# Performance work log

Hardware: AMD Instinct MI355X
Metric: run time of the kernel (lower is better)

Reference implementation:

```python
import jax, jax.numpy as jnp
import numpy as np

EPS = 1e-5
PI = np.pi
HPK_SCL = 4.0  # args.hpk_scl

def _nan_to(y, rep):
    return jnp.where(jnp.isnan(y), rep, y)

def _chi(x):
    return _nan_to(1.0 / jnp.sqrt(1.0 + PI * jnp.tan(x + EPS) ** 2), 0.0)

def _E1(x, th):
    return _nan_to(jnp.exp(-(2.0 / PI) / jnp.tan(th + EPS) / jnp.tan(x + EPS)), 0.0)

def _E2(x, th):
    return _nan_to(jnp.exp(-(1.0 / PI) * (1.0 / jnp.tan(th + EPS)) ** 2 * (1.0 / jnp.tan(x + EPS)) ** 2), 0.0)

def _eta(x, th):
    y = _chi(th) * (jnp.cos(x) + jnp.sin(x) * jnp.tan(th + EPS) * (_E2(x, th) / (2.0 - _E1(x, th))))
    return _nan_to(y, 0.0)

def _f(phi):
    return _nan_to(jnp.exp(-2.0 * jnp.tan((phi + EPS) / 2.0)), 0.0)

def _mu_eff(i, e, phi, th):
    E1i, E1e = _E1(i, th), _E1(e, th)
    E2i, E2e = _E2(i, th), _E2(e, th)
    sp2 = jnp.sin(phi / 2.0) ** 2
    y1 = (E2e - sp2 * E2i) / (2.0 - E1e - phi / PI * E1i)
    y2 = (jnp.cos(phi) * E2i + sp2 * E2e) / (2.0 - E1i - phi / PI * E1e)
    y = jnp.where(i <= e, y1, y2)
    y = _chi(th) * (jnp.cos(e) + jnp.sin(e) * jnp.tan(th) * y)
    return _nan_to(y, jnp.cos(e))

def _mu0_eff(i, e, phi, th):
    E1i, E1e = _E1(i, th), _E1(e, th)
    E2i, E2e = _E2(i, th), _E2(e, th)
    sp2 = jnp.sin(phi / 2.0) ** 2
    y1 = (jnp.cos(phi) * E2e + sp2 * E2i) / (2.0 - E1e - phi / PI * E1i)
    y2 = (E2i - sp2 * E2e) / (2.0 - E1i - phi / PI * E1e)
    y = jnp.where(i <= e, y1, y2)
    y = _chi(th) * (jnp.cos(i) + jnp.sin(i) * jnp.tan(th) * y)
    return _nan_to(y, jnp.cos(i))

def _S(i, e, phi, th):
    ci, cv = jnp.cos(i), jnp.cos(e)
    mue = _mu_eff(i, e, phi, th)
    etai, etae = _eta(i, th), _eta(e, th)
    chit = _chi(th)
    ff = _f(phi)
    temp = mue / etae * (ci / etai) * chit
    y = jnp.where(i <= e,
                  temp / (1.0 - ff + ff * chit * (ci / etai)),
                  temp / (1.0 - ff + ff * chit * (cv / etae)))
    return _nan_to(y, 0.0)

def _HF(x, w):
    gamma = jnp.sqrt(1.0 - w)
    ro = (1.0 - gamma) / (1.0 + gamma)
    log = jnp.log(jnp.abs((1.0 + x) / x))
    tmp1 = 1.0 - w * x * (ro + (1.0 - 2.0 * ro * x) / 2.0 * log)
    return _nan_to(1.0 / tmp1, 1.0)

def _PF(x, b, c):
    b2 = b ** 2
    bx = b * x
    y = c * (1.0 - b2) / (jnp.power(1.0 - 2.0 * bx + b2, 1.5) + 1e-6)
    y = y + (1.0 - c) * (1.0 - b2) / (jnp.power(1.0 + 2.0 * bx + b2, 1.5) + 1e-6)
    return _nan_to(y, 0.0)

def _normalize(x):
    return x / (jnp.linalg.norm(x, axis=-1, keepdims=True) + 1e-8)

def setup_inputs() -> dict:
    N = 1048576
    key = jax.random.key(0)
    ks = jax.random.split(key, 9)
    normal = _normalize(jax.random.normal(ks[0], (N, 3), dtype=jnp.float32))
    l = _normalize(jax.random.normal(ks[1], (N, 3), dtype=jnp.float32))
    l = l * jnp.where(jnp.sum(l * normal, -1, keepdims=True) >= 0, 1.0, -1.0)  # upper hemisphere
    v = _normalize(jax.random.normal(ks[2], (N, 3), dtype=jnp.float32))
    v = v * jnp.where(jnp.sum(v * normal, -1, keepdims=True) >= 0, 1.0, -1.0)
    return {
        'pts2l': l[:, None, :],
        'pts2c': v,
        'normal': normal,
        'w': 0.05 + 0.9 * jax.random.uniform(ks[3], (N, 3), dtype=jnp.float32),
        'b': 0.8 * jax.random.uniform(ks[4], (N, 3), dtype=jnp.float32),
        'c': jax.random.uniform(ks[5], (N, 3), dtype=jnp.float32),
        'theta': 0.05 + 0.5 * jax.random.uniform(ks[6], (N,), dtype=jnp.float32),
        'h': 0.05 + 0.5 * jax.random.uniform(ks[7], (N, 1), dtype=jnp.float32),
        'B0': jax.random.uniform(ks[8], (N, 1), dtype=jnp.float32),
    }

def reference(pts2l, pts2c, normal, w, b, c, theta, h, B0):
    l = pts2l[:, 0, :]
    v = pts2c
    # angles (basic_func.calc_angles)
    ci = jnp.clip(jnp.sum(normal * l, -1), -1.0, 1.0)   # cos(incidence)
    sza = jnp.arccos(ci)
    si = jnp.sin(sza)
    cv = jnp.clip(jnp.sum(normal * v, -1), -1.0, 1.0)   # cos(view)
    vza = jnp.arccos(cv)
    sv = jnp.sin(vza)
    cg = jnp.clip(jnp.sum(l * v, -1), -1.0, 1.0)        # cos(phase)
    g = jnp.arccos(cg)
    cphi = jnp.clip((cg - ci * cv) / (si * sv + 1e-8), -1.0, 1.0)
    phi = jnp.arccos(cphi)                              # relative azimuth

    P = _PF(cg[:, None], b, c)                          # [N,3] phase function
    B = B0 / (1.0 + (1.0 / h) * jnp.tan(g / 2.0)[:, None]) + 1.0  # [N,1] opposition surge

    ci_e = _mu0_eff(sza, vza, phi, theta)               # roughness-corrected cosines
    cv_e = _mu_eff(sza, vza, phi, theta)
    Shad = _S(sza, vza, phi, theta)[:, None]            # [N,1] shadowing

    Hi = _HF(ci_e[:, None], w)                          # Chandrasekhar H functions
    Hv = _HF(cv_e[:, None], w)

    tmp1 = (ci_e / (ci_e + cv_e) / jnp.cos(sza))[:, None]
    tmp2 = P * B + Hi * Hv - 1.0
    brdf = w / HPK_SCL * tmp1 * tmp2 * Shad
    return brdf
```

## Files before the change

### kernel.cpp

```cpp
#include <hip/hip_runtime.h>


#define PIF  3.14159265358979323846f
#define EPSF 1e-5f

__device__ __forceinline__ float rcp(float x)  { return __builtin_amdgcn_rcpf(x); }
__device__ __forceinline__ float rsq(float x)  { return __builtin_amdgcn_rsqf(x); }
__device__ __forceinline__ float sqf(float x)  { return __builtin_amdgcn_sqrtf(x); }
__device__ __forceinline__ float nz(float y, float r) { return (y != y) ? r : y; }
__device__ __forceinline__ float clamp1(float x) { return fminf(fmaxf(x, -1.0f), 1.0f); }
__device__ __forceinline__ float acos_poly(float x) {
    float a = fabsf(x);
    float r = sqf(1.0f - a) *
              (1.5707288f + a * (-0.2121144f + a * (0.0742610f + a * (-0.0187293f))));
    return (x >= 0.0f) ? r : (PIF - r);
}

__global__ __launch_bounds__(256)
void hapke_kernel(const float* __restrict__ pts2l, const float* __restrict__ pts2c,
                  const float* __restrict__ normal, const float* __restrict__ w,
                  const float* __restrict__ b, const float* __restrict__ c,
                  const float* __restrict__ theta, const float* __restrict__ h,
                  const float* __restrict__ B0, float* __restrict__ out, int N)
{
    int idx = blockIdx.x * blockDim.x + threadIdx.x;
    if (idx >= N) return;
    const int i3 = idx * 3;

    float lx = pts2l[i3], ly = pts2l[i3+1], lz = pts2l[i3+2];
    float vx = pts2c[i3], vy = pts2c[i3+1], vz = pts2c[i3+2];
    float nx = normal[i3], ny = normal[i3+1], nzc = normal[i3+2];

    float ci = clamp1(nx*lx + ny*ly + nzc*lz);
    float cv = clamp1(nx*vx + ny*vy + nzc*vz);
    float cg = clamp1(lx*vx + ly*vy + lz*vz);
    float si = sqf(1.0f - ci*ci);
    float sv = sqf(1.0f - cv*cv);
    float cphi = clamp1((cg - ci*cv) * rcp(si*sv + 1e-8f));
    float phipi = acos_poly(cphi) * (1.0f / PIF);

    float ffu = (1.0f - cphi) * rcp(1.0f + cphi);
    float ff  = (cphi <= -1.0f) ? __builtin_inff() : __expf(-2.0f * sqf(ffu));

    float th = theta[idx];
    float s = __sinf(th + EPSF), cth = __cosf(th + EPSF);
    float tt     = s * rcp(cth);
    float cot_th = cth * rcp(s);
    float cot_i  = ci * rcp(si);
    float cot_e  = cv * rcp(sv);

    float E1i = nz(__expf(-(2.0f/PIF) * cot_th * cot_i), 0.0f);
    float E1e = nz(__expf(-(2.0f/PIF) * cot_th * cot_e), 0.0f);
    float ct2 = cot_th * cot_th;
    float E2i = nz(__expf(-(1.0f/PIF) * ct2 * cot_i*cot_i), 0.0f);
    float E2e = nz(__expf(-(1.0f/PIF) * ct2 * cot_e*cot_e), 0.0f);

    float chit = rsq(1.0f + PIF * tt * tt);
    float etai = nz(chit * (ci + si * tt * (E2i * rcp(2.0f - E1i))), 0.0f);
    float etae = nz(chit * (cv + sv * tt * (E2e * rcp(2.0f - E1e))), 0.0f);

    float sp2 = 0.5f * (1.0f - cphi);
    bool  ile = (ci >= cv);
    float Ea  = ile ? E1e : E1i;
    float Eb  = ile ? E1i : E1e;
    float rd  = rcp(2.0f - Ea - phipi * Eb);
    float ymu  = (ile ? (E2e - sp2*E2i)       : (cphi*E2i + sp2*E2e)) * rd;
    float ymu0 = (ile ? (cphi*E2e + sp2*E2i)  : (E2i - sp2*E2e)) * rd;
    float cv_e = nz(chit * (cv + sv * tt * ymu ), cv);
    float ci_e = nz(chit * (ci + si * tt * ymu0), ci);

    float r_etai = rcp(etai), r_etae = rcp(etae);
    float ci_etai = ci * r_etai, cv_etae = cv * r_etae;
    float temp = cv_e * r_etae * ci_etai * chit;
    float den  = 1.0f - ff + ff * chit * (ile ? ci_etai : cv_etae);
    float shad = nz(temp * rcp(den), 0.0f);

    float tg2 = sqf((1.0f - cg) * rcp(1.0f + cg));
    float hh  = h[idx];
    float B   = B0[idx] * hh * rcp(hh + tg2) + 1.0f;
    float tmp1 = ci_e * rcp((ci_e + cv_e) * ci);

    float logi = 0.5f * __logf(fabsf((1.0f + ci_e) * rcp(ci_e)));
    float loge = 0.5f * __logf(fabsf((1.0f + cv_e) * rcp(cv_e)));

    #pragma unroll
    for (int k = 0; k < 3; ++k) {
        float wk = w[i3+k], bk = b[i3+k], ck = c[i3+k];
        float b2 = bk * bk, bx = bk * cg;
        float t1 = 1.0f - 2.0f*bx + b2;
        float t2 = 1.0f + 2.0f*bx + b2;
        float q1 = t1 * sqf(t1) + 1e-6f;
        float q2 = t2 * sqf(t2) + 1e-6f;
        float P  = (1.0f - b2) * (ck*q2 + (1.0f - ck)*q1) * rcp(q1*q2);
        float gamma = sqf(1.0f - wk);
        float ro = (1.0f - gamma) * rcp(1.0f + gamma);
        float Hi = nz(rcp(1.0f - wk*ci_e*(ro + (1.0f - 2.0f*ro*ci_e)*logi)), 1.0f);
        float Hv = nz(rcp(1.0f - wk*cv_e*(ro + (1.0f - 2.0f*ro*cv_e)*loge)), 1.0f);
        float tmp2 = P * B + Hi * Hv - 1.0f;
        out[i3+k] = wk * 0.25f * tmp1 * tmp2 * shad;
    }
}

extern "C" void kernel_launch(void* const* d_in, const int* in_sizes, int n_in,
                              void* d_out, int out_size, void* d_ws, size_t ws_size,
                              hipStream_t stream) {
    const float* pts2l  = (const float*)d_in[0];
    const float* pts2c  = (const float*)d_in[1];
    const float* normal = (const float*)d_in[2];
    const float* w      = (const float*)d_in[3];
    const float* b      = (const float*)d_in[4];
    const float* c      = (const float*)d_in[5];
    const float* theta  = (const float*)d_in[6];
    const float* h      = (const float*)d_in[7];
    const float* B0     = (const float*)d_in[8];
    float* out = (float*)d_out;

    int N = in_sizes[6];
    const int block = 256;
    int grid = (N + block - 1) / block;
    hapke_kernel<<<grid, block, 0, stream>>>(pts2l, pts2c, normal, w, b, c,
                                             theta, h, B0, out, N);
}
```

Before: 123.0 us.

## Process two points per thread with 8-byte vector loads and nontemporal stores

The per-point math moves into a device helper, and each thread now handles two consecutive points. The stride-3 arrays are read as three float2 loads per array and the per-point scalars as one float2, replacing scattered 4-byte loads with wider accesses. Outputs go out as three nontemporal float2 stores, and launch bounds add a 4-blocks hint. The grid is halved, which cuts thread count and per-thread parallelism in exchange for wider memory transactions and more register pressure.

```diff
diff --git a/kernel.cpp b/kernel.cpp
--- a/kernel.cpp
+++ b/kernel.cpp
@@ -3,6 +3,8 @@
 
 #define PIF  3.14159265358979323846f
 #define EPSF 1e-5f
+
+typedef float v2f __attribute__((ext_vector_type(2)));
 
 __device__ __forceinline__ float rcp(float x)  { return __builtin_amdgcn_rcpf(x); }
 __device__ __forceinline__ float rsq(float x)  { return __builtin_amdgcn_rsqf(x); }
@@ -16,38 +18,32 @@
     return (x >= 0.0f) ? r : (PIF - r);
 }
 
-__global__ __launch_bounds__(256)
-void hapke_kernel(const float* __restrict__ pts2l, const float* __restrict__ pts2c,
-                  const float* __restrict__ normal, const float* __restrict__ w,
-                  const float* __restrict__ b, const float* __restrict__ c,
-                  const float* __restrict__ theta, const float* __restrict__ h,
-                  const float* __restrict__ B0, float* __restrict__ out, int N)
+__device__ __forceinline__ void hapke_point(
+    float lx, float ly, float lz,
+    float vx, float vy, float vz,
+    float nx, float ny, float nzc,
+    float th, float hh, float B0v,
+    float w0, float w1, float w2,
+    float b0, float b1, float b2,
+    float c0, float c1, float c2,
+    float outv[3])
 {
-    int idx = blockIdx.x * blockDim.x + threadIdx.x;
-    if (idx >= N) return;
-    const int i3 = idx * 3;
-
-    float lx = pts2l[i3], ly = pts2l[i3+1], lz = pts2l[i3+2];
-    float vx = pts2c[i3], vy = pts2c[i3+1], vz = pts2c[i3+2];
-    float nx = normal[i3], ny = normal[i3+1], nzc = normal[i3+2];
-
-    float ci = clamp1(nx*lx + ny*ly + nzc*lz);
-    float cv = clamp1(nx*vx + ny*vy + nzc*vz);
-    float cg = clamp1(lx*vx + ly*vy + lz*vz);
-    float si = sqf(1.0f - ci*ci);
-    float sv = sqf(1.0f - cv*cv);
-    float cphi = clamp1((cg - ci*cv) * rcp(si*sv + 1e-8f));
+    float ci  = clamp1(nx*lx + ny*ly + nzc*lz);
+    float cvv = clamp1(nx*vx + ny*vy + nzc*vz);
+    float cg  = clamp1(lx*vx + ly*vy + lz*vz);
+    float si  = sqf(1.0f - ci*ci);
+    float sv  = sqf(1.0f - cvv*cvv);
+    float cphi = clamp1((cg - ci*cvv) * rcp(si*sv + 1e-8f));
     float phipi = acos_poly(cphi) * (1.0f / PIF);
 
     float ffu = (1.0f - cphi) * rcp(1.0f + cphi);
     float ff  = (cphi <= -1.0f) ? __builtin_inff() : __expf(-2.0f * sqf(ffu));
 
-    float th = theta[idx];
     float s = __sinf(th + EPSF), cth = __cosf(th + EPSF);
     float tt     = s * rcp(cth);
     float cot_th = cth * rcp(s);
     float cot_i  = ci * rcp(si);
-    float cot_e  = cv * rcp(sv);
+    float cot_e  = cvv * rcp(sv);
 
     float E1i = nz(__expf(-(2.0f/PIF) * cot_th * cot_i), 0.0f);
     float E1e = nz(__expf(-(2.0f/PIF) * cot_th * cot_e), 0.0f);
@@ -56,36 +52,38 @@
     float E2e = nz(__expf(-(1.0f/PIF) * ct2 * cot_e*cot_e), 0.0f);
 
     float chit = rsq(1.0f + PIF * tt * tt);
-    float etai = nz(chit * (ci + si * tt * (E2i * rcp(2.0f - E1i))), 0.0f);
-    float etae = nz(chit * (cv + sv * tt * (E2e * rcp(2.0f - E1e))), 0.0f);
+    float etai = nz(chit * (ci  + si * tt * (E2i * rcp(2.0f - E1i))), 0.0f);
+    float etae = nz(chit * (cvv + sv * tt * (E2e * rcp(2.0f - E1e))), 0.0f);
 
     float sp2 = 0.5f * (1.0f - cphi);
-    bool  ile = (ci >= cv);
+    bool  ile = (ci >= cvv);
     float Ea  = ile ? E1e : E1i;
     float Eb  = ile ? E1i : E1e;
     float rd  = rcp(2.0f - Ea - phipi * Eb);
-    float ymu  = (ile ? (E2e - sp2*E2i)       : (cphi*E2i + sp2*E2e)) * rd;
-    float ymu0 = (ile ? (cphi*E2e + sp2*E2i)  : (E2i - sp2*E2e)) * rd;
-    float cv_e = nz(chit * (cv + sv * tt * ymu ), cv);
-    float ci_e = nz(chit * (ci + si * tt * ymu0), ci);
+    float ymu  = (ile ? (E2e - sp2*E2i)      : (cphi*E2i + sp2*E2e)) * rd;
+    float ymu0 = (ile ? (cphi*E2e + sp2*E2i) : (E2i - sp2*E2e)) * rd;
+    float cv_e = nz(chit * (cvv + sv * tt * ymu ), cvv);
+    float ci_e = nz(chit * (ci  + si * tt * ymu0), ci);
 
     float r_etai = rcp(etai), r_etae = rcp(etae);
-    float ci_etai = ci * r_etai, cv_etae = cv * r_etae;
+    float ci_etai = ci * r_etai, cv_etae = cvv * r_etae;
     float temp = cv_e * r_etae * ci_etai * chit;
     float den  = 1.0f - ff + ff * chit * (ile ? ci_etai : cv_etae);
     float shad = nz(temp * rcp(den), 0.0f);
 
     float tg2 = sqf((1.0f - cg) * rcp(1.0f + cg));
-    float hh  = h[idx];
-    float B   = B0[idx] * hh * rcp(hh + tg2) + 1.0f;
+    float B   = B0v * hh * rcp(hh + tg2) + 1.0f;
     float tmp1 = ci_e * rcp((ci_e + cv_e) * ci);
 
     float logi = 0.5f * __logf(fabsf((1.0f + ci_e) * rcp(ci_e)));
     float loge = 0.5f * __logf(fabsf((1.0f + cv_e) * rcp(cv_e)));
 
+    const float wk3[3] = {w0, w1, w2};
+    const float bk3[3] = {b0, b1, b2};
+    const float ck3[3] = {c0, c1, c2};
     #pragma unroll
     for (int k = 0; k < 3; ++k) {
-        float wk = w[i3+k], bk = b[i3+k], ck = c[i3+k];
+        float wk = wk3[k], bk = bk3[k], ck = ck3[k];
         float b2 = bk * bk, bx = bk * cg;
         float t1 = 1.0f - 2.0f*bx + b2;
         float t2 = 1.0f + 2.0f*bx + b2;
@@ -97,7 +95,67 @@
         float Hi = nz(rcp(1.0f - wk*ci_e*(ro + (1.0f - 2.0f*ro*ci_e)*logi)), 1.0f);
         float Hv = nz(rcp(1.0f - wk*cv_e*(ro + (1.0f - 2.0f*ro*cv_e)*loge)), 1.0f);
         float tmp2 = P * B + Hi * Hv - 1.0f;
-        out[i3+k] = wk * 0.25f * tmp1 * tmp2 * shad;
+        outv[k] = wk * 0.25f * tmp1 * tmp2 * shad;
+    }
+}
+
+__global__ __launch_bounds__(256, 4)
+void hapke_kernel(const float* __restrict__ pts2l, const float* __restrict__ pts2c,
+                  const float* __restrict__ normal, const float* __restrict__ w,
+                  const float* __restrict__ b, const float* __restrict__ c,
+                  const float* __restrict__ theta, const float* __restrict__ h,
+                  const float* __restrict__ B0, float* __restrict__ out, int N)
+{
+    int t  = blockIdx.x * blockDim.x + threadIdx.x;
+    int p0 = t * 2;
+    if (p0 >= N) return;
+
+    if (p0 + 1 < N) {
+        const v2f* L2 = (const v2f*)pts2l;
+        const v2f* V2 = (const v2f*)pts2c;
+        const v2f* N2 = (const v2f*)normal;
+        const v2f* W2 = (const v2f*)w;
+        const v2f* Bb2 = (const v2f*)b;
+        const v2f* C2 = (const v2f*)c;
+        const v2f* T2 = (const v2f*)theta;
+        const v2f* H2 = (const v2f*)h;
+        const v2f* Z2 = (const v2f*)B0;
+
+        int t3 = 3 * t;
+        v2f la = L2[t3], lb = L2[t3+1], lc = L2[t3+2];
+        v2f va = V2[t3], vb = V2[t3+1], vc = V2[t3+2];
+        v2f na = N2[t3], nb = N2[t3+1], nc = N2[t3+2];
+        v2f wa = W2[t3], wb = W2[t3+1], wc = W2[t3+2];
+        v2f ba = Bb2[t3], bb = Bb2[t3+1], bc = Bb2[t3+2];
+        v2f ca = C2[t3], cb = C2[t3+1], cc = C2[t3+2];
+        v2f th2 = T2[t], h2 = H2[t], z2 = Z2[t];
+
+        float oA[3], oB[3];
+        hapke_point(la.x, la.y, lb.x,  va.x, va.y, vb.x,  na.x, na.y, nb.x,
+                    th2.x, h2.x, z2.x,
+                    wa.x, wa.y, wb.x,  ba.x, ba.y, bb.x,  ca.x, ca.y, cb.x, oA);
+        hapke_point(lb.y, lc.x, lc.y,  vb.y, vc.x, vc.y,  nb.y, nc.x, nc.y,
+                    th2.y, h2.y, z2.y,
+                    wb.y, wc.x, wc.y,  bb.y, bc.x, bc.y,  cb.y, cc.x, cc.y, oB);
+
+        v2f* O2 = (v2f*)out;
+        v2f s0; s0.x = oA[0]; s0.y = oA[1];
+        v2f s1; s1.x = oA[2]; s1.y = oB[0];
+        v2f s2; s2.x = oB[1]; s2.y = oB[2];
+        __builtin_nontemporal_store(s0, &O2[t3]);
+        __builtin_nontemporal_store(s1, &O2[t3+1]);
+        __builtin_nontemporal_store(s2, &O2[t3+2]);
+    } else {
+        int i3 = p0 * 3;
+        float oA[3];
+        hapke_point(pts2l[i3], pts2l[i3+1], pts2l[i3+2],
+                    pts2c[i3], pts2c[i3+1], pts2c[i3+2],
+                    normal[i3], normal[i3+1], normal[i3+2],
+                    theta[p0], h[p0], B0[p0],
+                    w[i3], w[i3+1], w[i3+2],
+                    b[i3], b[i3+1], b[i3+2],
+                    c[i3], c[i3+1], c[i3+2], oA);
+        out[i3] = oA[0]; out[i3+1] = oA[1]; out[i3+2] = oA[2];
     }
 }
 
@@ -117,7 +175,8 @@
 
     int N = in_sizes[6];
     const int block = 256;
-    int grid = (N + block - 1) / block;
+    int nthreads = (N + 1) / 2;
+    int grid = (nthreads + block - 1) / block;
     hapke_kernel<<<grid, block, 0, stream>>>(pts2l, pts2c, normal, w, b, c,
                                              theta, h, B0, out, N);
 }
```

Measured after the change: 123.3 us, median of 2. About the same (+0.2%).
